# Optimization experiments

Hardware: AMD Instinct MI355X
Metric: run time of the kernel (lower is better)

The kernel has to match this reference:

```python
import jax, jax.numpy as jnp
import numpy as np

NTIME = 20      # number of time blocks
V = 128         # vehicle_num per time block
F_OUT = 128     # out_features (== in_features here)
ALPHA = 0.2     # LeakyReLU negative slope
NEG = -9e15     # mask fill value used by the torch module


def setup_inputs() -> dict:
    key = jax.random.key(0)
    k1, k2, k3, k4 = jax.random.split(key, 4)
    h = jax.random.normal(k1, (NTIME * V, F_OUT), dtype=jnp.float32)
    # binary adjacency mask, broadcast over the feature dim like the torch code
    adj = jax.random.randint(k2, (V, V, 1), 0, 2).astype(jnp.float32)
    share_weight = jax.random.normal(k3, (F_OUT, F_OUT), dtype=jnp.float32) * 0.05
    a = jax.random.normal(k4, (2 * F_OUT, F_OUT), dtype=jnp.float32) * 0.05
    return {"h": h, "adj": adj, "share_weight": share_weight, "a": a}


def reference(h, adj, share_weight, a):
    # Wh: [N, F]
    Wh = h @ share_weight
    # a_input @ a decomposes: e[p,q,:] = leakyrelu(Wh[p] @ a[:F] + Wh[q] @ a[F:])
    # Only the block-diagonal (per-time) slices of e are ever used, so compute
    # blocks directly instead of the full NxNxF tensor.
    a1, a2 = a[:F_OUT], a[F_OUT:]
    e1 = (Wh @ a1).reshape(NTIME, V, F_OUT)  # [T, v, F]
    e2 = (Wh @ a2).reshape(NTIME, V, F_OUT)
    e = e1[:, :, None, :] + e2[:, None, :, :]           # [T, v, v, F]
    e = jnp.where(e > 0, e, ALPHA * e)                   # LeakyReLU
    masked = jnp.where(adj[None] > 0, e, NEG)            # mask per time block
    # torch softmax(dim=1) on [v, v, F] blocks -> axis=2 here (the j index)
    attention_raw = jax.nn.softmax(masked, axis=2)       # [T, v, v, F]
    # training=False => dropout is identity.
    # h_prime[t,b,f] = sum_j att[t,b,j,f] * Wh[t,j,f]  (the diagonal-of-matmul trick)
    Whb = Wh.reshape(NTIME, V, F_OUT)
    h_prime = jnp.einsum('tbjf,tjf->tbf', attention_raw, Whb)
    out = jax.nn.elu(h_prime)                            # concat=True branch
    return (out, attention_raw)
```

## Files before the change

kernel.cpp:

```cpp
#include <hip/hip_runtime.h>
#include <math.h>

#define NTIME 20
#define V 128
#define F 128
constexpr float ALPHA = 0.2f;

typedef float f32x4 __attribute__((ext_vector_type(4)));

__global__ __launch_bounds__(128) void k_wa(const float* __restrict__ W,
                                            const float* __restrict__ a,
                                            float* __restrict__ Wa) {
  const int i = blockIdx.x;
  const int s = blockIdx.y;
  const int k = threadIdx.x;
  __shared__ float wrow[F];
  wrow[k] = W[i * F + k];
  __syncthreads();
  const float* as = a + s * F * F;
  float acc = 0.f;
#pragma unroll 8
  for (int m = 0; m < F; ++m) acc += wrow[m] * as[m * F + k];
  Wa[(s * F + i) * F + k] = acc;
}

__global__ __launch_bounds__(256) void k_gemm(const float* __restrict__ h,
                                              const float* __restrict__ W,
                                              const float* __restrict__ Wa,
                                              float* __restrict__ Wh,
                                              float* __restrict__ E1,
                                              float* __restrict__ E2) {
  __shared__ float Alds[32][129];
  __shared__ float Blds[128][64];
  const int tid = threadIdx.x;
  const int rb = blockIdx.x * 32;
  const int matc = blockIdx.y >> 1;
  const int cb = (blockIdx.y & 1) * 64;

#pragma unroll
  for (int p = 0; p < 4; ++p) {
    int id = tid + p * 256;
    int row = id >> 5;
    int c0 = (id & 31) * 4;
    float4 v = *reinterpret_cast<const float4*>(&h[(rb + row) * F + c0]);
    Alds[row][c0 + 0] = v.x; Alds[row][c0 + 1] = v.y;
    Alds[row][c0 + 2] = v.z; Alds[row][c0 + 3] = v.w;
  }
  const float* src = (matc == 0) ? W : (Wa + (matc - 1) * F * F);
#pragma unroll
  for (int p = 0; p < 8; ++p) {
    int id = tid + p * 256;
    int k = id >> 4;
    int c0 = (id & 15) * 4;
    float4 v = *reinterpret_cast<const float4*>(&src[k * F + cb + c0]);
    Blds[k][c0 + 0] = v.x; Blds[k][c0 + 1] = v.y;
    Blds[k][c0 + 2] = v.z; Blds[k][c0 + 3] = v.w;
  }
  __syncthreads();

  const int tx = tid & 15;
  const int ty = tid >> 4;
  float acc[2][4] = {};
#pragma unroll 4
  for (int k = 0; k < 128; ++k) {
    float4 bv = *reinterpret_cast<const float4*>(&Blds[k][tx * 4]);
    float a0 = Alds[ty * 2 + 0][k];
    float a1 = Alds[ty * 2 + 1][k];
    acc[0][0] += a0 * bv.x; acc[0][1] += a0 * bv.y; acc[0][2] += a0 * bv.z; acc[0][3] += a0 * bv.w;
    acc[1][0] += a1 * bv.x; acc[1][1] += a1 * bv.y; acc[1][2] += a1 * bv.z; acc[1][3] += a1 * bv.w;
  }

  float* Dp = (matc == 0) ? Wh : ((matc == 1) ? E1 : E2);
  const int gr0 = rb + ty * 2;
  const int c0 = cb + tx * 4;
#pragma unroll
  for (int i = 0; i < 2; ++i) {
    float4 v;
    v.x = acc[i][0]; v.y = acc[i][1]; v.z = acc[i][2]; v.w = acc[i][3];
    *reinterpret_cast<float4*>(&Dp[(gr0 + i) * F + c0]) = v;
  }
}

__global__ __launch_bounds__(256, 5) void k_attn(const float* __restrict__ Wh,
                                                 const float* __restrict__ E1,
                                                 const float* __restrict__ E2,
                                                 const float* __restrict__ adj,
                                                 float* __restrict__ out,
                                                 float* __restrict__ att) {
  __shared__ float sA[2][4][F];
  __shared__ float hA[2][4][F];
  __shared__ float invA[2][F];
  __shared__ float uniA[2];

  const int r0 = blockIdx.x * 2;
  const int r1 = r0 + 1;
  const int t = r0 >> 7;
  const int b0 = r0 & 127;
  const int w = threadIdx.x >> 6;
  const int lane = threadIdx.x & 63;
  const int fc = lane * 2;
  const int j0 = w * 32;

  const float* E2t = E2 + t * V * F;
  const float* Wht = Wh + t * V * F;
  const float* adj0 = adj + b0 * V;
  const float* adj1 = adj0 + V;

  const bool in32 = lane < 32;
  const unsigned long long Ma = __ballot(in32 ? (adj0[j0 + (lane & 31)] > 0.f) : false);
  const unsigned long long Mb = __ballot(in32 ? (adj1[j0 + (lane & 31)] > 0.f) : false);
  const unsigned ma32 = (unsigned)Ma;
  const unsigned mb32 = (unsigned)Mb;

  const float2 e1a = *reinterpret_cast<const float2*>(E1 + r0 * F + fc);
  const float2 e1b = *reinterpret_cast<const float2*>(E1 + r1 * F + fc);

  float sa0 = 0.f, sa1 = 0.f, ha0 = 0.f, ha1 = 0.f;
  float sb0 = 0.f, sb1 = 0.f, hb0 = 0.f, hb1 = 0.f;
#pragma unroll 8
  for (int jj = 0; jj < 32; ++jj) {
    const int j = j0 + jj;
    const float2 e2 = *reinterpret_cast<const float2*>(E2t + j * F + fc);
    const float2 wv = *reinterpret_cast<const float2*>(Wht + j * F + fc);
    const float ga = (float)((ma32 >> jj) & 1u);
    const float gb = (float)((mb32 >> jj) & 1u);
    float x0 = e1a.x + e2.x, x1 = e1a.y + e2.y;
    x0 = fmaxf(x0, ALPHA * x0);
    x1 = fmaxf(x1, ALPHA * x1);
    float p0 = __expf(x0) * ga, p1 = __expf(x1) * ga;
    sa0 += p0; sa1 += p1;
    ha0 = fmaf(p0, wv.x, ha0); ha1 = fmaf(p1, wv.y, ha1);
    x0 = e1b.x + e2.x; x1 = e1b.y + e2.y;
    x0 = fmaxf(x0, ALPHA * x0);
    x1 = fmaxf(x1, ALPHA * x1);
    p0 = __expf(x0) * gb; p1 = __expf(x1) * gb;
    sb0 += p0; sb1 += p1;
    hb0 = fmaf(p0, wv.x, hb0); hb1 = fmaf(p1, wv.y, hb1);
  }
  sA[0][w][fc] = sa0; sA[0][w][fc + 1] = sa1;
  hA[0][w][fc] = ha0; hA[0][w][fc + 1] = ha1;
  sA[1][w][fc] = sb0; sA[1][w][fc + 1] = sb1;
  hA[1][w][fc] = hb0; hA[1][w][fc + 1] = hb1;
  __syncthreads();

  if (w < 2) {
    const int row = w;
    const int r = r0 + row;
    const float S0 = sA[row][0][fc] + sA[row][1][fc] + sA[row][2][fc] + sA[row][3][fc];
    const float S1 = sA[row][0][fc + 1] + sA[row][1][fc + 1] + sA[row][2][fc + 1] + sA[row][3][fc + 1];
    const bool uni = (S0 == 0.f);
    const float inv0 = uni ? (1.f / (float)V) : (1.f / S0);
    const float inv1 = uni ? (1.f / (float)V) : (1.f / S1);
    invA[row][fc] = inv0; invA[row][fc + 1] = inv1;
    if (lane == 0) uniA[row] = uni ? 1.f : 0.f;

    float H0, H1;
    if (uni) {
      H0 = 0.f; H1 = 0.f;
      for (int j = 0; j < V; ++j) {
        float2 wv = *reinterpret_cast<const float2*>(Wht + j * F + fc);
        H0 += wv.x; H1 += wv.y;
      }
      H0 *= inv0; H1 *= inv1;
    } else {
      H0 = (hA[row][0][fc] + hA[row][1][fc] + hA[row][2][fc] + hA[row][3][fc]) * inv0;
      H1 = (hA[row][0][fc + 1] + hA[row][1][fc + 1] + hA[row][2][fc + 1] + hA[row][3][fc + 1]) * inv1;
    }
    float2 ov;
    ov.x = H0 > 0.f ? H0 : __expf(H0) - 1.f;
    ov.y = H1 > 0.f ? H1 : __expf(H1) - 1.f;
    *reinterpret_cast<float2*>(out + r * F + fc) = ov;
  }
  __syncthreads();

  const int jh = lane >> 5;
  const int f4 = (lane & 31) * 4;
  const float4 e1qa = *reinterpret_cast<const float4*>(E1 + r0 * F + f4);
  const float4 e1qb = *reinterpret_cast<const float4*>(E1 + r1 * F + f4);
  const float4 invqa = *reinterpret_cast<const float4*>(&invA[0][f4]);
  const float4 invqb = *reinterpret_cast<const float4*>(&invA[1][f4]);
  const bool ua = uniA[0] != 0.f;
  const bool ub = uniA[1] != 0.f;
  float* attb0 = att + (size_t)r0 * (V * F);
  float* attb1 = att + (size_t)r1 * (V * F);
  const unsigned maL = ma32 >> jh;
  const unsigned mbL = mb32 >> jh;

  if (!(ua | ub)) {
#pragma unroll 4
    for (int jj = 0; jj < 16; ++jj) {
      const int j = j0 + jj * 2 + jh;
      const float4 e2q = *reinterpret_cast<const float4*>(E2t + j * F + f4);
      const float ga = (float)((maL >> (2 * jj)) & 1u);
      const float gb = (float)((mbL >> (2 * jj)) & 1u);
      const float va0 = invqa.x * ga, va1 = invqa.y * ga, va2 = invqa.z * ga, va3 = invqa.w * ga;
      const float vb0 = invqb.x * gb, vb1 = invqb.y * gb, vb2 = invqb.z * gb, vb3 = invqb.w * gb;

      float x0 = e1qa.x + e2q.x, x1 = e1qa.y + e2q.y;
      float x2 = e1qa.z + e2q.z, x3 = e1qa.w + e2q.w;
      x0 = fmaxf(x0, ALPHA * x0); x1 = fmaxf(x1, ALPHA * x1);
      x2 = fmaxf(x2, ALPHA * x2); x3 = fmaxf(x3, ALPHA * x3);
      f32x4 o;
      o.x = __expf(x0) * va0; o.y = __expf(x1) * va1;
      o.z = __expf(x2) * va2; o.w = __expf(x3) * va3;
      __builtin_nontemporal_store(o, reinterpret_cast<f32x4*>(attb0 + j * F + f4));

      x0 = e1qb.x + e2q.x; x1 = e1qb.y + e2q.y;
      x2 = e1qb.z + e2q.z; x3 = e1qb.w + e2q.w;
      x0 = fmaxf(x0, ALPHA * x0); x1 = fmaxf(x1, ALPHA * x1);
      x2 = fmaxf(x2, ALPHA * x2); x3 = fmaxf(x3, ALPHA * x3);
      o.x = __expf(x0) * vb0; o.y = __expf(x1) * vb1;
      o.z = __expf(x2) * vb2; o.w = __expf(x3) * vb3;
      __builtin_nontemporal_store(o, reinterpret_cast<f32x4*>(attb1 + j * F + f4));
    }
  } else {
#pragma unroll 2
    for (int jj = 0; jj < 16; ++jj) {
      const int j = j0 + jj * 2 + jh;
      const float4 e2q = *reinterpret_cast<const float4*>(E2t + j * F + f4);
      const float ga = (float)((maL >> (2 * jj)) & 1u);
      const float gb = (float)((mbL >> (2 * jj)) & 1u);
      {
        float x0 = e1qa.x + e2q.x, x1 = e1qa.y + e2q.y;
        float x2 = e1qa.z + e2q.z, x3 = e1qa.w + e2q.w;
        x0 = fmaxf(x0, ALPHA * x0); x1 = fmaxf(x1, ALPHA * x1);
        x2 = fmaxf(x2, ALPHA * x2); x3 = fmaxf(x3, ALPHA * x3);
        float4 o;
        o.x = __expf(x0) * invqa.x * ga; o.y = __expf(x1) * invqa.y * ga;
        o.z = __expf(x2) * invqa.z * ga; o.w = __expf(x3) * invqa.w * ga;
        if (ua) { o.x = invqa.x; o.y = invqa.y; o.z = invqa.z; o.w = invqa.w; }
        *reinterpret_cast<float4*>(attb0 + j * F + f4) = o;
      }
      {
        float x0 = e1qb.x + e2q.x, x1 = e1qb.y + e2q.y;
        float x2 = e1qb.z + e2q.z, x3 = e1qb.w + e2q.w;
        x0 = fmaxf(x0, ALPHA * x0); x1 = fmaxf(x1, ALPHA * x1);
        x2 = fmaxf(x2, ALPHA * x2); x3 = fmaxf(x3, ALPHA * x3);
        float4 o;
        o.x = __expf(x0) * invqb.x * gb; o.y = __expf(x1) * invqb.y * gb;
        o.z = __expf(x2) * invqb.z * gb; o.w = __expf(x3) * invqb.w * gb;
        if (ub) { o.x = invqb.x; o.y = invqb.y; o.z = invqb.z; o.w = invqb.w; }
        *reinterpret_cast<float4*>(attb1 + j * F + f4) = o;
      }
    }
  }
}

extern "C" void kernel_launch(void* const* d_in, const int* in_sizes, int n_in,
                              void* d_out, int out_size, void* d_ws, size_t ws_size,
                              hipStream_t stream) {
  (void)in_sizes; (void)n_in; (void)out_size; (void)ws_size;
  const float* h   = (const float*)d_in[0];
  const float* adj = (const float*)d_in[1];
  const float* W   = (const float*)d_in[2];
  const float* a   = (const float*)d_in[3];

  float* Wh = (float*)d_ws;
  float* E1 = Wh + NTIME * V * F;
  float* E2 = E1 + NTIME * V * F;
  float* Wa = E2 + NTIME * V * F;

  float* out = (float*)d_out;
  float* att = out + NTIME * V * F;

  k_wa<<<dim3(128, 2), 128, 0, stream>>>(W, a, Wa);
  k_gemm<<<dim3(80, 6), 256, 0, stream>>>(h, W, Wa, Wh, E1, E2);
  k_attn<<<dim3(NTIME * V / 2), 256, 0, stream>>>(Wh, E1, E2, adj, out, att);
}
```

Before: 199.3 us.

## Compute E from Wh directly and fold log2e into E to use exp2

Replaces the W·a precompute plus single combined GEMM with two dependent GEMM launches, Wh = h·W followed by E1/E2 = Wh·a. The log2(e) factor is folded into the a tile when it is staged into shared memory, so the attention kernel can call exp2f directly instead of __expf. Because LeakyReLU is positively homogeneous, this scaling stays exact up to rounding. The cost is two serialized GEMM launches instead of one, and the E GEMM must wait for Wh.

```diff
diff --git a/kernel.cpp b/kernel.cpp
--- a/kernel.cpp
+++ b/kernel.cpp
@@ -5,56 +5,36 @@
 #define V 128
 #define F 128
 constexpr float ALPHA = 0.2f;
+constexpr float LOG2E = 1.44269504088896340736f;
 
 typedef float f32x4 __attribute__((ext_vector_type(4)));
 
-__global__ __launch_bounds__(128) void k_wa(const float* __restrict__ W,
-                                            const float* __restrict__ a,
-                                            float* __restrict__ Wa) {
-  const int i = blockIdx.x;
-  const int s = blockIdx.y;
-  const int k = threadIdx.x;
-  __shared__ float wrow[F];
-  wrow[k] = W[i * F + k];
-  __syncthreads();
-  const float* as = a + s * F * F;
-  float acc = 0.f;
-#pragma unroll 8
-  for (int m = 0; m < F; ++m) acc += wrow[m] * as[m * F + k];
-  Wa[(s * F + i) * F + k] = acc;
-}
-
-__global__ __launch_bounds__(256) void k_gemm(const float* __restrict__ h,
-                                              const float* __restrict__ W,
-                                              const float* __restrict__ Wa,
-                                              float* __restrict__ Wh,
-                                              float* __restrict__ E1,
-                                              float* __restrict__ E2) {
+__device__ __forceinline__ void gemm_tile(const float* __restrict__ A,
+                                          const float* __restrict__ B,
+                                          float* __restrict__ D,
+                                          const int rb, const int cb,
+                                          const float bscale) {
   __shared__ float Alds[32][129];
   __shared__ float Blds[128][64];
   const int tid = threadIdx.x;
-  const int rb = blockIdx.x * 32;
-  const int matc = blockIdx.y >> 1;
-  const int cb = (blockIdx.y & 1) * 64;
 
 #pragma unroll
   for (int p = 0; p < 4; ++p) {
     int id = tid + p * 256;
     int row = id >> 5;
     int c0 = (id & 31) * 4;
-    float4 v = *reinterpret_cast<const float4*>(&h[(rb + row) * F + c0]);
+    float4 v = *reinterpret_cast<const float4*>(&A[(rb + row) * F + c0]);
     Alds[row][c0 + 0] = v.x; Alds[row][c0 + 1] = v.y;
     Alds[row][c0 + 2] = v.z; Alds[row][c0 + 3] = v.w;
   }
-  const float* src = (matc == 0) ? W : (Wa + (matc - 1) * F * F);
 #pragma unroll
   for (int p = 0; p < 8; ++p) {
     int id = tid + p * 256;
     int k = id >> 4;
     int c0 = (id & 15) * 4;
-    float4 v = *reinterpret_cast<const float4*>(&src[k * F + cb + c0]);
-    Blds[k][c0 + 0] = v.x; Blds[k][c0 + 1] = v.y;
-    Blds[k][c0 + 2] = v.z; Blds[k][c0 + 3] = v.w;
+    float4 v = *reinterpret_cast<const float4*>(&B[k * F + cb + c0]);
+    Blds[k][c0 + 0] = v.x * bscale; Blds[k][c0 + 1] = v.y * bscale;
+    Blds[k][c0 + 2] = v.z * bscale; Blds[k][c0 + 3] = v.w * bscale;
   }
   __syncthreads();
 
@@ -70,15 +50,29 @@
     acc[1][0] += a1 * bv.x; acc[1][1] += a1 * bv.y; acc[1][2] += a1 * bv.z; acc[1][3] += a1 * bv.w;
   }
 
-  float* Dp = (matc == 0) ? Wh : ((matc == 1) ? E1 : E2);
   const int gr0 = rb + ty * 2;
   const int c0 = cb + tx * 4;
 #pragma unroll
   for (int i = 0; i < 2; ++i) {
     float4 v;
     v.x = acc[i][0]; v.y = acc[i][1]; v.z = acc[i][2]; v.w = acc[i][3];
-    *reinterpret_cast<float4*>(&Dp[(gr0 + i) * F + c0]) = v;
-  }
+    *reinterpret_cast<float4*>(&D[(gr0 + i) * F + c0]) = v;
+  }
+}
+
+__global__ __launch_bounds__(256) void k_wh(const float* __restrict__ h,
+                                            const float* __restrict__ W,
+                                            float* __restrict__ Wh) {
+  gemm_tile(h, W, Wh, blockIdx.x * 32, blockIdx.y * 64, 1.0f);
+}
+
+__global__ __launch_bounds__(256) void k_e(const float* __restrict__ Wh,
+                                           const float* __restrict__ a,
+                                           float* __restrict__ E1,
+                                           float* __restrict__ E2) {
+  const int mat = blockIdx.y >> 1;
+  gemm_tile(Wh, a + mat * F * F, mat ? E2 : E1,
+            blockIdx.x * 32, (blockIdx.y & 1) * 64, LOG2E);
 }
 
 __global__ __launch_bounds__(256, 5) void k_attn(const float* __restrict__ Wh,
@@ -127,13 +121,13 @@
     float x0 = e1a.x + e2.x, x1 = e1a.y + e2.y;
     x0 = fmaxf(x0, ALPHA * x0);
     x1 = fmaxf(x1, ALPHA * x1);
-    float p0 = __expf(x0) * ga, p1 = __expf(x1) * ga;
+    float p0 = exp2f(x0) * ga, p1 = exp2f(x1) * ga;
     sa0 += p0; sa1 += p1;
     ha0 = fmaf(p0, wv.x, ha0); ha1 = fmaf(p1, wv.y, ha1);
     x0 = e1b.x + e2.x; x1 = e1b.y + e2.y;
     x0 = fmaxf(x0, ALPHA * x0);
     x1 = fmaxf(x1, ALPHA * x1);
-    p0 = __expf(x0) * gb; p1 = __expf(x1) * gb;
+    p0 = exp2f(x0) * gb; p1 = exp2f(x1) * gb;
     sb0 += p0; sb1 += p1;
     hb0 = fmaf(p0, wv.x, hb0); hb1 = fmaf(p1, wv.y, hb1);
   }
@@ -201,16 +195,16 @@
       x0 = fmaxf(x0, ALPHA * x0); x1 = fmaxf(x1, ALPHA * x1);
       x2 = fmaxf(x2, ALPHA * x2); x3 = fmaxf(x3, ALPHA * x3);
       f32x4 o;
-      o.x = __expf(x0) * va0; o.y = __expf(x1) * va1;
-      o.z = __expf(x2) * va2; o.w = __expf(x3) * va3;
+      o.x = exp2f(x0) * va0; o.y = exp2f(x1) * va1;
+      o.z = exp2f(x2) * va2; o.w = exp2f(x3) * va3;
       __builtin_nontemporal_store(o, reinterpret_cast<f32x4*>(attb0 + j * F + f4));
 
       x0 = e1qb.x + e2q.x; x1 = e1qb.y + e2q.y;
       x2 = e1qb.z + e2q.z; x3 = e1qb.w + e2q.w;
       x0 = fmaxf(x0, ALPHA * x0); x1 = fmaxf(x1, ALPHA * x1);
       x2 = fmaxf(x2, ALPHA * x2); x3 = fmaxf(x3, ALPHA * x3);
-      o.x = __expf(x0) * vb0; o.y = __expf(x1) * vb1;
-      o.z = __expf(x2) * vb2; o.w = __expf(x3) * vb3;
+      o.x = exp2f(x0) * vb0; o.y = exp2f(x1) * vb1;
+      o.z = exp2f(x2) * vb2; o.w = exp2f(x3) * vb3;
       __builtin_nontemporal_store(o, reinterpret_cast<f32x4*>(attb1 + j * F + f4));
     }
   } else {
@@ -226,8 +220,8 @@
         x0 = fmaxf(x0, ALPHA * x0); x1 = fmaxf(x1, ALPHA * x1);
         x2 = fmaxf(x2, ALPHA * x2); x3 = fmaxf(x3, ALPHA * x3);
         float4 o;
-        o.x = __expf(x0) * invqa.x * ga; o.y = __expf(x1) * invqa.y * ga;
-        o.z = __expf(x2) * invqa.z * ga; o.w = __expf(x3) * invqa.w * ga;
+        o.x = exp2f(x0) * invqa.x * ga; o.y = exp2f(x1) * invqa.y * ga;
+        o.z = exp2f(x2) * invqa.z * ga; o.w = exp2f(x3) * invqa.w * ga;
         if (ua) { o.x = invqa.x; o.y = invqa.y; o.z = invqa.z; o.w = invqa.w; }
         *reinterpret_cast<float4*>(attb0 + j * F + f4) = o;
       }
@@ -237,8 +231,8 @@
         x0 = fmaxf(x0, ALPHA * x0); x1 = fmaxf(x1, ALPHA * x1);
         x2 = fmaxf(x2, ALPHA * x2); x3 = fmaxf(x3, ALPHA * x3);
         float4 o;
-        o.x = __expf(x0) * invqb.x * gb; o.y = __expf(x1) * invqb.y * gb;
-        o.z = __expf(x2) * invqb.z * gb; o.w = __expf(x3) * invqb.w * gb;
+        o.x = exp2f(x0) * invqb.x * gb; o.y = exp2f(x1) * invqb.y * gb;
+        o.z = exp2f(x2) * invqb.z * gb; o.w = exp2f(x3) * invqb.w * gb;
         if (ub) { o.x = invqb.x; o.y = invqb.y; o.z = invqb.z; o.w = invqb.w; }
         *reinterpret_cast<float4*>(attb1 + j * F + f4) = o;
       }
@@ -258,12 +252,11 @@
   float* Wh = (float*)d_ws;
   float* E1 = Wh + NTIME * V * F;
   float* E2 = E1 + NTIME * V * F;
-  float* Wa = E2 + NTIME * V * F;
 
   float* out = (float*)d_out;
   float* att = out + NTIME * V * F;
 
-  k_wa<<<dim3(128, 2), 128, 0, stream>>>(W, a, Wa);
-  k_gemm<<<dim3(80, 6), 256, 0, stream>>>(h, W, Wa, Wh, E1, E2);
+  k_wh<<<dim3(80, 2), 256, 0, stream>>>(h, W, Wh);
+  k_e<<<dim3(80, 4), 256, 0, stream>>>(Wh, a, E1, E2);
   k_attn<<<dim3(NTIME * V / 2), 256, 0, stream>>>(Wh, E1, E2, adj, out, att);
 }
```

Measured after the change: 209.2 us. 1.05x slower.
